# Kernel optimization log

Measured on AMD Instinct MI355X. Metric: run time of the kernel, lower is better.

## Reference

```python
import jax, jax.numpy as jnp
import numpy as np

LAYER_SIZES = [1024, 1024, 1024, 1024, 1024, 1024, 512]
MAX_PATHS = 128
BATCH = 128
N_LAYERS = len(LAYER_SIZES) - 1


def setup_inputs() -> dict:
    key = jax.random.key(0)
    keys = jax.random.split(key, 1 + 2 * N_LAYERS)
    inp = {"x": jax.random.normal(keys[0], (BATCH, LAYER_SIZES[0]), dtype=jnp.float32)}
    for i in range(N_LAYERS):
        inp[f"W{i}"] = jax.random.normal(keys[1 + 2 * i], (LAYER_SIZES[i], LAYER_SIZES[i + 1]), dtype=jnp.float32) * 0.01
        inp[f"b{i}"] = jax.random.normal(keys[2 + 2 * i], (LAYER_SIZES[i + 1],), dtype=jnp.float32) * 0.01
    return inp


def _layer(data, W, b):
    # data: [B, in_feat, P] -> [B, out_feat, 3P]
    B, _, P = data.shape
    O = W.shape[1]
    pos = jnp.einsum('bfp,fo->bpo', data, W) + b          # [B, P, O]; neg branch is exactly -pos
    branches = jnp.stack([-pos, jnp.zeros_like(pos), pos], axis=-1)  # [B, P, O, 3]
    # transpose(1,2) then reshape: interleave branches per source path, matching torch
    return branches.transpose(0, 2, 1, 3).reshape(B, O, P * 3)


def _prune(data, keep):
    # keep top-`keep` paths by L2 norm over the feature dim
    norms = jnp.linalg.norm(data, axis=1)                 # [B, P]
    _, idx = jax.lax.top_k(norms, keep)                   # [B, keep]
    return jnp.take_along_axis(data, idx[:, None, :], axis=-1)


def _forward(x, Ws, bs):
    data = x[:, :, None]                                   # [B, F, 1]
    for i in range(N_LAYERS):
        data = _layer(data, Ws[i], bs[i])
        if i < N_LAYERS - 1:
            data = jnp.tanh(data)
        if data.shape[-1] > MAX_PATHS:
            data = _prune(data, MAX_PATHS)
    # collapse with 'max_abs': per (batch, feature) pick path with largest |value|
    idx = jnp.argmax(jnp.abs(data), axis=-1, keepdims=True)
    output = jnp.take_along_axis(data, idx, axis=-1).squeeze(-1)
    return output, data


def reference(x, W0, b0, W1, b1, W2, b2, W3, b3, W4, b4, W5, b5):
    Ws = [W0, W1, W2, W3, W4, W5]
    bs = [b0, b1, b2, b3, b4, b5]
    return _forward(x, Ws, bs)
```

## Files before the change

### kernel.cpp

```cpp
#include <hip/hip_runtime.h>
#include <math.h>


using s8v = __attribute__((ext_vector_type(8))) short;
using f4v = __attribute__((ext_vector_type(4))) float;

__device__ __forceinline__ float bf2f(short b) {
  unsigned u = ((unsigned)(unsigned short)b) << 16;
  return __builtin_bit_cast(float, u);
}
__device__ __forceinline__ short f2bf(float f) {
  unsigned u = __builtin_bit_cast(unsigned, f);
  u = (u + 0x7FFFu + ((u >> 16) & 1u)) >> 16;
  return (short)u;
}
__device__ __forceinline__ void split_store(float f, short* hi, short* lo) {
  short h = f2bf(f);
  *hi = h;
  *lo = f2bf(f - bf2f(h));
}

__global__ void __launch_bounds__(256)
packx_k(const float* __restrict__ x, short* __restrict__ hi,
        short* __restrict__ lo) {
  int i = (blockIdx.x * 256 + threadIdx.x) * 4;
  float4 v = *(const float4*)&x[i];
  short4 h, l;
  h.x = f2bf(v.x); l.x = f2bf(v.x - bf2f(h.x));
  h.y = f2bf(v.y); l.y = f2bf(v.y - bf2f(h.y));
  h.z = f2bf(v.z); l.z = f2bf(v.z - bf2f(h.z));
  h.w = f2bf(v.w); l.w = f2bf(v.w - bf2f(h.w));
  *(short4*)&hi[i] = h;
  *(short4*)&lo[i] = l;
}

struct TWArgs {
  const float* W[6];
  short* Th[6];
  short* Tl[6];
};
__global__ void __launch_bounds__(256)
transW_all(TWArgs a) {
  const int z = blockIdx.z;
  const int N = (z == 5) ? 512 : 1024;
  const int n0 = blockIdx.x * 64, k0 = blockIdx.y * 64;
  if (n0 >= N) return;
  const float* __restrict__ W = a.W[z];
  short* __restrict__ Th = a.Th[z];
  short* __restrict__ Tl = a.Tl[z];
  __shared__ float tile[64][65];
  const int t = threadIdx.x;
  const int r = t >> 4, c4 = (t & 15) * 4;
#pragma unroll
  for (int i = 0; i < 4; ++i) {
    int rr = r + 16 * i;
    float4 v = *(const float4*)&W[(size_t)(k0 + rr) * N + n0 + c4];
    tile[rr][c4 + 0] = v.x;
    tile[rr][c4 + 1] = v.y;
    tile[rr][c4 + 2] = v.z;
    tile[rr][c4 + 3] = v.w;
  }
  __syncthreads();
#pragma unroll
  for (int i = 0; i < 4; ++i) {
    int n = r + 16 * i;
    short4 h, l;
    float f0 = tile[c4 + 0][n], f1 = tile[c4 + 1][n];
    float f2 = tile[c4 + 2][n], f3 = tile[c4 + 3][n];
    h.x = f2bf(f0); l.x = f2bf(f0 - bf2f(h.x));
    h.y = f2bf(f1); l.y = f2bf(f1 - bf2f(h.y));
    h.z = f2bf(f2); l.z = f2bf(f2 - bf2f(h.z));
    h.w = f2bf(f3); l.w = f2bf(f3 - bf2f(h.w));
    size_t o = (size_t)(n0 + n) * 1024 + k0 + c4;
    *(short4*)&Th[o] = h;
    *(short4*)&Tl[o] = l;
  }
}

template <int MODE, int D, int KS>
__global__ void __launch_bounds__(256, 2)
mfma_gemm(const short* __restrict__ Ah, const short* __restrict__ Al,
          const short* __restrict__ Bh, const short* __restrict__ Bl,
          const float* __restrict__ bias, short* __restrict__ Oh,
          short* __restrict__ Ol, float* __restrict__ Of, int N, int Dn) {
  constexpr int KC = 1024 / KS;
  constexpr int BKP = 40;
  __shared__ short As_h[64 * BKP], As_l[64 * BKP];
  __shared__ short Bs_h[64 * BKP], Bs_l[64 * BKP];
  const int t = threadIdx.x;
  const int row0 = blockIdx.y * 64;
  const int col0 = blockIdx.x * 64;
  const int kb = blockIdx.z * KC;
  const int sr = t >> 2, sko = (t & 3) * 8;
  const short* Ahp = Ah + (size_t)(row0 + sr) * 1024 + kb + sko;
  const short* Alp = Al + (size_t)(row0 + sr) * 1024 + kb + sko;
  const short* Bhp = Bh + (size_t)(col0 + sr) * 1024 + kb + sko;
  const short* Blp = Bl + (size_t)(col0 + sr) * 1024 + kb + sko;
  const int w = t >> 6, lane = t & 63;
  const int l16 = lane & 15, q = lane >> 4;
  const int wm0 = (w & 1) * 32, wn0 = (w >> 1) * 32;
  const int abase = (wm0 + l16) * BKP + q * 8;
  const int bbase = (wn0 + l16) * BKP + q * 8;
  f4v acc[2][2];
#pragma unroll
  for (int i = 0; i < 2; ++i)
#pragma unroll
    for (int j = 0; j < 2; ++j) acc[i][j] = (f4v){0.f, 0.f, 0.f, 0.f};
  uint4 rah = *(const uint4*)(Ahp);
  uint4 ral = *(const uint4*)(Alp);
  uint4 rbh = *(const uint4*)(Bhp);
  uint4 rbl = *(const uint4*)(Blp);
  for (int k0 = 0; k0 < KC; k0 += 32) {
    __syncthreads();
    *(uint4*)&As_h[sr * BKP + sko] = rah;
    *(uint4*)&As_l[sr * BKP + sko] = ral;
    *(uint4*)&Bs_h[sr * BKP + sko] = rbh;
    *(uint4*)&Bs_l[sr * BKP + sko] = rbl;
    if (k0 + 32 < KC) {
      rah = *(const uint4*)(Ahp + k0 + 32);
      ral = *(const uint4*)(Alp + k0 + 32);
      rbh = *(const uint4*)(Bhp + k0 + 32);
      rbl = *(const uint4*)(Blp + k0 + 32);
    }
    __syncthreads();
    s8v ah[2], al[2], bh[2], bl[2];
#pragma unroll
    for (int mt = 0; mt < 2; ++mt) {
      ah[mt] = *(const s8v*)&As_h[abase + mt * 16 * BKP];
      al[mt] = *(const s8v*)&As_l[abase + mt * 16 * BKP];
    }
#pragma unroll
    for (int nt = 0; nt < 2; ++nt) {
      bh[nt] = *(const s8v*)&Bs_h[bbase + nt * 16 * BKP];
      bl[nt] = *(const s8v*)&Bs_l[bbase + nt * 16 * BKP];
    }
#pragma unroll
    for (int mt = 0; mt < 2; ++mt)
#pragma unroll
      for (int nt = 0; nt < 2; ++nt) {
        acc[mt][nt] = __builtin_amdgcn_mfma_f32_16x16x32_bf16(
            ah[mt], bh[nt], acc[mt][nt], 0, 0, 0);
        acc[mt][nt] = __builtin_amdgcn_mfma_f32_16x16x32_bf16(
            ah[mt], bl[nt], acc[mt][nt], 0, 0, 0);
        acc[mt][nt] = __builtin_amdgcn_mfma_f32_16x16x32_bf16(
            al[mt], bh[nt], acc[mt][nt], 0, 0, 0);
      }
  }
  const int R = (int)gridDim.y << 6;
#pragma unroll
  for (int nt = 0; nt < 2; ++nt) {
    int gcol = col0 + wn0 + nt * 16 + l16;
    float bc = (MODE == 1) ? bias[gcol] : 0.f;
#pragma unroll
    for (int mt = 0; mt < 2; ++mt) {
#pragma unroll
      for (int r = 0; r < 4; ++r) {
        float v = acc[mt][nt][r];
        int rr = row0 + wm0 + mt * 16 + q * 4 + r;
        if (MODE == 1) {
          int b = rr / D, u = rr - b * D;
          size_t ob = (size_t)(b * Dn) * N + gcol;
          size_t om = ob + (size_t)(1 + 2 * u) * N;
          size_t op = ob + (size_t)(2 + 2 * u) * N;
          split_store(tanhf(bc - v), &Oh[om], &Ol[om]);
          split_store(tanhf(bc + v), &Oh[op], &Ol[op]);
          if (u == 0) split_store(tanhf(bc), &Oh[ob], &Ol[ob]);
        } else if (MODE == 2) {
          Of[(size_t)rr * N + gcol] = v;
        } else {
          Of[((size_t)blockIdx.z * R + rr) * N + gcol] = v;
        }
      }
    }
  }
}

template <int KS>
__global__ void __launch_bounds__(256)
comb0_hl(const float* __restrict__ P, const float* __restrict__ bias,
         short* __restrict__ Oh, short* __restrict__ Ol, int R, int N) {
  int i = blockIdx.x * 256 + threadIdx.x;
  int n4 = N >> 2;
  int r = i / n4, c4 = (i - r * n4) * 4;
  float4 y = *(const float4*)&P[(size_t)r * N + c4];
  size_t stride = (size_t)R * N;
#pragma unroll
  for (int ks = 1; ks < KS; ++ks) {
    const float4 p = *(const float4*)&P[ks * stride + (size_t)r * N + c4];
    y.x += p.x; y.y += p.y; y.z += p.z; y.w += p.w;
  }
  float4 bc = *(const float4*)(bias + c4);
  float t0 = tanhf(bc.x + y.x), t1 = tanhf(bc.y + y.y);
  float t2 = tanhf(bc.z + y.z), t3 = tanhf(bc.w + y.w);
  short4 h, l;
  h.x = f2bf(t0); l.x = f2bf(t0 - bf2f(h.x));
  h.y = f2bf(t1); l.y = f2bf(t1 - bf2f(h.y));
  h.z = f2bf(t2); l.z = f2bf(t2 - bf2f(h.z));
  h.w = f2bf(t3); l.w = f2bf(t3 - bf2f(h.w));
  *(short4*)&Oh[(size_t)r * N + c4] = h;
  *(short4*)&Ol[(size_t)r * N + c4] = l;
}

template <int KS, int D>
__global__ void __launch_bounds__(256)
comb1_hl(const float* __restrict__ P, const float* __restrict__ bias,
         short* __restrict__ Oh, short* __restrict__ Ol, int R, int N,
         int Dn) {
  int i = blockIdx.x * 256 + threadIdx.x;
  int n4 = N >> 2;
  int r = i / n4, c4 = (i - r * n4) * 4;
  int b = r / D, u = r - b * D;
  float4 y = *(const float4*)&P[(size_t)r * N + c4];
  size_t stride = (size_t)R * N;
#pragma unroll
  for (int ks = 1; ks < KS; ++ks) {
    const float4 p = *(const float4*)&P[ks * stride + (size_t)r * N + c4];
    y.x += p.x; y.y += p.y; y.z += p.z; y.w += p.w;
  }
  float4 bc = *(const float4*)(bias + c4);
  size_t ob = (size_t)(b * Dn) * N + c4;
  size_t om = ob + (size_t)(1 + 2 * u) * N;
  size_t op = ob + (size_t)(2 + 2 * u) * N;
  {
    float t0 = tanhf(bc.x - y.x), t1 = tanhf(bc.y - y.y);
    float t2 = tanhf(bc.z - y.z), t3 = tanhf(bc.w - y.w);
    short4 h, l;
    h.x = f2bf(t0); l.x = f2bf(t0 - bf2f(h.x));
    h.y = f2bf(t1); l.y = f2bf(t1 - bf2f(h.y));
    h.z = f2bf(t2); l.z = f2bf(t2 - bf2f(h.z));
    h.w = f2bf(t3); l.w = f2bf(t3 - bf2f(h.w));
    *(short4*)&Oh[om] = h;
    *(short4*)&Ol[om] = l;
  }
  {
    float t0 = tanhf(bc.x + y.x), t1 = tanhf(bc.y + y.y);
    float t2 = tanhf(bc.z + y.z), t3 = tanhf(bc.w + y.w);
    short4 h, l;
    h.x = f2bf(t0); l.x = f2bf(t0 - bf2f(h.x));
    h.y = f2bf(t1); l.y = f2bf(t1 - bf2f(h.y));
    h.z = f2bf(t2); l.z = f2bf(t2 - bf2f(h.z));
    h.w = f2bf(t3); l.w = f2bf(t3 - bf2f(h.w));
    *(short4*)&Oh[op] = h;
    *(short4*)&Ol[op] = l;
  }
  if (u == 0) {
    float t0 = tanhf(bc.x), t1 = tanhf(bc.y);
    float t2 = tanhf(bc.z), t3 = tanhf(bc.w);
    short4 h, l;
    h.x = f2bf(t0); l.x = f2bf(t0 - bf2f(h.x));
    h.y = f2bf(t1); l.y = f2bf(t1 - bf2f(h.y));
    h.z = f2bf(t2); l.z = f2bf(t2 - bf2f(h.z));
    h.w = f2bf(t3); l.w = f2bf(t3 - bf2f(h.w));
    *(short4*)&Oh[ob] = h;
    *(short4*)&Ol[ob] = l;
  }
}

__global__ void __launch_bounds__(256)
rownorm_hl(const short* __restrict__ hi, const short* __restrict__ lo,
           float* __restrict__ ns) {
  int row = blockIdx.x;
  int t = threadIdx.x;
  size_t base = (size_t)row * 1024 + t * 4;
  short4 h = *(const short4*)&hi[base];
  short4 l = *(const short4*)&lo[base];
  float v0 = bf2f(h.x) + bf2f(l.x);
  float v1 = bf2f(h.y) + bf2f(l.y);
  float v2 = bf2f(h.z) + bf2f(l.z);
  float v3 = bf2f(h.w) + bf2f(l.w);
  float s = v0 * v0 + v1 * v1 + v2 * v2 + v3 * v3;
  __shared__ float red[256];
  red[t] = s;
  __syncthreads();
  for (int off = 128; off; off >>= 1) {
    if (t < off) red[t] += red[t + off];
    __syncthreads();
  }
  if (t == 0) ns[row] = red[0];
}

__global__ void __launch_bounds__(256)
prune4_k(const float* __restrict__ ns, int* __restrict__ kept4) {
  int b = blockIdx.x, t = threadIdx.x;
  __shared__ float nss[31];
  __shared__ float key[243];
  __shared__ int cls[243];
  if (t < 31) nss[t] = ns[b * 31 + t];
  __syncthreads();
  if (t < 243) {
    int j = t / 3, t4 = t - 3 * j;
    int d0 = j / 27, d1 = (j / 9) % 3, d2 = (j / 3) % 3, d3 = j % 3;
    int u = 0;
    u = (d0 == 1) ? 0 : (1 + 2 * u + (d0 == 2));
    u = (d1 == 1) ? 0 : (1 + 2 * u + (d1 == 2));
    u = (d2 == 1) ? 0 : (1 + 2 * u + (d2 == 2));
    u = (d3 == 1) ? 0 : (1 + 2 * u + (d3 == 2));
    cls[t] = u;
    key[t] = (t4 == 1) ? 0.f : nss[u];
  }
  __syncthreads();
  if (t < 243) {
    float k = key[t];
    int rank = 0;
    for (int e = 0; e < 243; ++e) {
      float ke = key[e];
      rank += (ke > k) || (ke == k && e < t);
    }
    if (rank < 128) {
      int t4 = t - 3 * (t / 3);
      kept4[b * 128 + rank] = (cls[t] << 1) | (t4 == 2 ? 1 : 0);
    }
  }
}

__global__ void __launch_bounds__(256)
stats5_k(const float* __restrict__ Y5, const float* __restrict__ b5,
         float* __restrict__ dotv, float* __restrict__ nrmv,
         float* __restrict__ nb5) {
  int row = blockIdx.x;
  int t = threadIdx.x;
  __shared__ float rd[256], rn[256];
  if (row < 3968) {
    const float* y = Y5 + (size_t)row * 512;
    float d = 0.f, n2 = 0.f;
    for (int o = t; o < 512; o += 256) {
      float v = y[o];
      d = fmaf(b5[o], v, d);
      n2 = fmaf(v, v, n2);
    }
    rd[t] = d;
    rn[t] = n2;
    __syncthreads();
    for (int off = 128; off; off >>= 1) {
      if (t < off) {
        rd[t] += rd[t + off];
        rn[t] += rn[t + off];
      }
      __syncthreads();
    }
    if (t == 0) {
      dotv[row] = rd[0];
      nrmv[row] = rn[0];
    }
  } else {
    float n2 = 0.f;
    for (int o = t; o < 512; o += 256) {
      float v = b5[o];
      n2 = fmaf(v, v, n2);
    }
    rn[t] = n2;
    __syncthreads();
    for (int off = 128; off; off >>= 1) {
      if (t < off) rn[t] += rn[t + off];
      __syncthreads();
    }
    if (t == 0) nb5[0] = rn[0];
  }
}

__global__ void __launch_bounds__(384)
prune5_k(const float* __restrict__ dotv, const float* __restrict__ nrmv,
         const float* __restrict__ nb5, const int* __restrict__ kept4,
         int* __restrict__ kept5) {
  int b = blockIdx.x, t = threadIdx.x;
  __shared__ float pns[128];
  __shared__ float key[384];
  if (t < 128) {
    int k4 = kept4[b * 128 + t];
    int c = k4 >> 1;
    float s = (k4 & 1) ? 1.f : -1.f;
    pns[t] = nb5[0] + nrmv[b * 31 + c] + s * 2.f * dotv[b * 31 + c];
  }
  __syncthreads();
  int m = t / 3, tt = t - 3 * m;
  key[t] = (tt == 1) ? 0.f : pns[m];
  __syncthreads();
  float k = key[t];
  int rank = 0;
  for (int e = 0; e < 384; ++e) {
    float ke = key[e];
    rank += (ke > k) || (ke == k && e < t);
  }
  if (rank < 128) kept5[b * 128 + rank] = (m << 1) | (tt == 2 ? 1 : 0);
}

__global__ void __launch_bounds__(256)
finalize_k(const float* __restrict__ Y5, const float* __restrict__ b5,
           const int* __restrict__ kept4, const int* __restrict__ kept5,
           float* __restrict__ out, float* __restrict__ dataout) {
  const int b = blockIdx.y;
  const int o0 = blockIdx.x * 64;
  __shared__ float Ys[31][65];
  __shared__ float bias_s[64];
  __shared__ float vt[64][130];
  __shared__ float ra[64][4];
  __shared__ float rv[64][4];
  const int t = threadIdx.x;
  for (int idx = t; idx < 31 * 64; idx += 256) {
    int c = idx >> 6, o = idx & 63;
    Ys[c][o] = Y5[((size_t)b * 31 + c) * 512 + o0 + o];
  }
  if (t < 64) bias_s[t] = b5[o0 + t];
  const int rr = t & 127, oh = t >> 7;
  int k5 = kept5[b * 128 + rr];
  int m = k5 >> 1;
  float sig = (k5 & 1) ? 1.f : -1.f;
  int k4 = kept4[b * 128 + m];
  int cc = k4 >> 1;
  float s4 = (k4 & 1) ? 1.f : -1.f;
  float afac = sig * s4;
  __syncthreads();
#pragma unroll
  for (int ol = 0; ol < 32; ++ol) {
    int o = oh * 32 + ol;
    float v = sig * bias_s[o] + afac * Ys[cc][o];
    dataout[((size_t)b * 512 + o0 + o) * 128 + rr] = v;
    vt[o][rr] = v;
  }
  __syncthreads();
  int o = t >> 2, q = t & 3;
  float bestv = vt[o][q * 32];
  float besta = fabsf(bestv);
  for (int i = 1; i < 32; ++i) {
    float v = vt[o][q * 32 + i];
    float a = fabsf(v);
    if (a > besta) {
      besta = a;
      bestv = v;
    }
  }
  ra[o][q] = besta;
  rv[o][q] = bestv;
  __syncthreads();
  if (t < 64) {
    float ba = ra[t][0], bv = rv[t][0];
#pragma unroll
    for (int qq = 1; qq < 4; ++qq) {
      if (ra[t][qq] > ba) {
        ba = ra[t][qq];
        bv = rv[t][qq];
      }
    }
    out[(size_t)b * 512 + o0 + t] = bv;
  }
}

extern "C" void kernel_launch(void* const* d_in, const int* in_sizes, int n_in,
                              void* d_out, int out_size, void* d_ws,
                              size_t ws_size, hipStream_t stream) {
  const float* x = (const float*)d_in[0];
  const float* Wt[6];
  const float* bs[6];
  for (int i = 0; i < 6; ++i) {
    Wt[i] = (const float*)d_in[1 + 2 * i];
    bs[i] = (const float*)d_in[2 + 2 * i];
  }
  char* base = (char*)d_ws;
  short* A0h = (short*)(base + 0);
  short* A0l = (short*)(base + 262144);
  short* Wh[6], *Wl[6];
  {
    size_t off = 524288;
    for (int i = 0; i < 6; ++i) {
      size_t sz = (i < 5) ? 2097152 : 1048576;
      Wh[i] = (short*)(base + off);
      Wl[i] = (short*)(base + off + sz);
      off += 2 * sz;
    }
  }
  short* C1h = (short*)(base + 23592960), *C1l = (short*)(base + 23855104);
  short* C2h = (short*)(base + 24117248), *C2l = (short*)(base + 24903680);
  short* C3h = (short*)(base + 25690112), *C3l = (short*)(base + 27525120);
  short* C4h = (short*)(base + 29360128), *C4l = (short*)(base + 33292288);
  short* C5h = (short*)(base + 524288);
  short* C5l = (short*)(base + 8912896);
  float* PA = (float*)(base + 29360128);
  float* PB = (float*)(base + 524288);
  float* Y5 = (float*)(base + 23592960);
  float* ns = (float*)(base + 37224448);
  float* dotv = (float*)(base + 37240320);
  float* nrmv = (float*)(base + 37256192);
  float* nb5 = (float*)(base + 37272064);
  int* kept4 = (int*)(base + 37272068);
  int* kept5 = (int*)(base + 37337604);
  float* outp = (float*)d_out;
  float* dataout = outp + 128 * 512;

  dim3 blk(256);
  packx_k<<<dim3(128), blk, 0, stream>>>(x, A0h, A0l);
  TWArgs twa;
  for (int i = 0; i < 6; ++i) {
    twa.W[i] = Wt[i];
    twa.Th[i] = Wh[i];
    twa.Tl[i] = Wl[i];
  }
  transW_all<<<dim3(16, 16, 6), blk, 0, stream>>>(twa);

  mfma_gemm<3, 1, 4><<<dim3(16, 2, 4), blk, 0, stream>>>(
      A0h, A0l, Wh[0], Wl[0], nullptr, nullptr, nullptr, PA, 1024, 0);
  comb0_hl<4><<<dim3(128), blk, 0, stream>>>(PA, bs[0], C1h, C1l, 128, 1024);
  mfma_gemm<3, 1, 4><<<dim3(16, 2, 4), blk, 0, stream>>>(
      C1h, C1l, Wh[1], Wl[1], nullptr, nullptr, nullptr, PA, 1024, 0);
  comb1_hl<4, 1><<<dim3(128), blk, 0, stream>>>(PA, bs[1], C2h, C2l, 128, 1024,
                                                3);
  mfma_gemm<3, 3, 4><<<dim3(16, 6, 4), blk, 0, stream>>>(
      C2h, C2l, Wh[2], Wl[2], nullptr, nullptr, nullptr, PA, 1024, 0);
  comb1_hl<4, 3><<<dim3(384), blk, 0, stream>>>(PA, bs[2], C3h, C3l, 384, 1024,
                                                7);
  mfma_gemm<3, 7, 2><<<dim3(16, 14, 2), blk, 0, stream>>>(
      C3h, C3l, Wh[3], Wl[3], nullptr, nullptr, nullptr, PB, 1024, 0);
  comb1_hl<2, 7><<<dim3(896), blk, 0, stream>>>(PB, bs[3], C4h, C4l, 896, 1024,
                                                15);
  mfma_gemm<1, 15, 1><<<dim3(16, 30), blk, 0, stream>>>(
      C4h, C4l, Wh[4], Wl[4], bs[4], C5h, C5l, nullptr, 1024, 31);
  rownorm_hl<<<dim3(3968), blk, 0, stream>>>(C5h, C5l, ns);
  prune4_k<<<dim3(128), blk, 0, stream>>>(ns, kept4);
  mfma_gemm<2, 31, 1><<<dim3(8, 62), blk, 0, stream>>>(
      C5h, C5l, Wh[5], Wl[5], nullptr, nullptr, nullptr, Y5, 512, 0);
  stats5_k<<<dim3(3969), blk, 0, stream>>>(Y5, bs[5], dotv, nrmv, nb5);
  prune5_k<<<dim3(128), dim3(384), 0, stream>>>(dotv, nrmv, nb5, kept4, kept5);
  finalize_k<<<dim3(8, 128), blk, 0, stream>>>(Y5, bs[5], kept4, kept5, outp,
                                               dataout);
}
```

Baseline: 243.1 us.

## Fuse split-K reductions, row norms and stats into GEMM epilogues

Folds the x packing and zeroing of counters/accumulators into the weight-transpose launch. Split-K partial reductions with bias+tanh+hi/lo split now run inside the GEMM, done by the last-arriving block per tile via an atomic counter; layer 0/1 split-K is raised to 8. Row norms and the layer-5 dot/norm stats are computed in the GEMM epilogues with shuffle reductions and float atomics, and the two prune kernels are merged into one. This removes about seven launches and their intermediate global round trips, at the cost of atomics, thread fences and nondeterministic float summation order.

Result: slower. 421.3 us (+73.3%).

```diff
diff --git a/kernel.cpp b/kernel.cpp
--- a/kernel.cpp
+++ b/kernel.cpp
@@ -18,20 +18,6 @@
   short h = f2bf(f);
   *hi = h;
   *lo = f2bf(f - bf2f(h));
-}
-
-__global__ void __launch_bounds__(256)
-packx_k(const float* __restrict__ x, short* __restrict__ hi,
-        short* __restrict__ lo) {
-  int i = (blockIdx.x * 256 + threadIdx.x) * 4;
-  float4 v = *(const float4*)&x[i];
-  short4 h, l;
-  h.x = f2bf(v.x); l.x = f2bf(v.x - bf2f(h.x));
-  h.y = f2bf(v.y); l.y = f2bf(v.y - bf2f(h.y));
-  h.z = f2bf(v.z); l.z = f2bf(v.z - bf2f(h.z));
-  h.w = f2bf(v.w); l.w = f2bf(v.w - bf2f(h.w));
-  *(short4*)&hi[i] = h;
-  *(short4*)&lo[i] = l;
 }
 
 struct TWArgs {
@@ -40,7 +26,31 @@
   short* Tl[6];
 };
 __global__ void __launch_bounds__(256)
-transW_all(TWArgs a) {
+transW_all(TWArgs a, const float* __restrict__ x, short* __restrict__ A0h,
+           short* __restrict__ A0l, float4* __restrict__ zreg) {
+  __shared__ float tile[64][65];
+  const int t = threadIdx.x;
+  if (blockIdx.z == 6) {
+    const int bf = blockIdx.y * 16 + blockIdx.x;
+    if (bf < 128) {
+      int i = (bf * 256 + t) * 4;
+      float4 v = *(const float4*)&x[i];
+      short4 h, l;
+      h.x = f2bf(v.x); l.x = f2bf(v.x - bf2f(h.x));
+      h.y = f2bf(v.y); l.y = f2bf(v.y - bf2f(h.y));
+      h.z = f2bf(v.z); l.z = f2bf(v.z - bf2f(h.z));
+      h.w = f2bf(v.w); l.w = f2bf(v.w - bf2f(h.w));
+      *(short4*)&A0h[i] = h;
+      *(short4*)&A0l[i] = l;
+    } else {
+      int flat = (bf - 128) * 256 + t;
+      if (flat < 3168) {
+        float4 zz = {0.f, 0.f, 0.f, 0.f};
+        zreg[flat] = zz;
+      }
+    }
+    return;
+  }
   const int z = blockIdx.z;
   const int N = (z == 5) ? 512 : 1024;
   const int n0 = blockIdx.x * 64, k0 = blockIdx.y * 64;
@@ -48,8 +58,6 @@
   const float* __restrict__ W = a.W[z];
   short* __restrict__ Th = a.Th[z];
   short* __restrict__ Tl = a.Tl[z];
-  __shared__ float tile[64][65];
-  const int t = threadIdx.x;
   const int r = t >> 4, c4 = (t & 15) * 4;
 #pragma unroll
   for (int i = 0; i < 4; ++i) {
@@ -82,7 +90,9 @@
 mfma_gemm(const short* __restrict__ Ah, const short* __restrict__ Al,
           const short* __restrict__ Bh, const short* __restrict__ Bl,
           const float* __restrict__ bias, short* __restrict__ Oh,
-          short* __restrict__ Ol, float* __restrict__ Of, int N, int Dn) {
+          short* __restrict__ Ol, float* __restrict__ Of,
+          float* __restrict__ aux0, float* __restrict__ aux1,
+          int* __restrict__ cnt, int N, int Dn) {
   constexpr int KC = 1024 / KS;
   constexpr int BKP = 40;
   __shared__ short As_h[64 * BKP], As_l[64 * BKP];
@@ -147,146 +157,194 @@
       }
   }
   const int R = (int)gridDim.y << 6;
+
+  if (MODE == 1) {
+    const float bc0 = bias[col0 + wn0 + l16];
+    const float bc1 = bias[col0 + wn0 + 16 + l16];
+#pragma unroll
+    for (int mt = 0; mt < 2; ++mt) {
+#pragma unroll
+      for (int r = 0; r < 4; ++r) {
+        const int rr = row0 + wm0 + mt * 16 + q * 4 + r;
+        const int b = rr / D, u = rr - b * D;
+        const size_t obr = (size_t)(b * Dn) * N;
+        const size_t omr = obr + (size_t)(1 + 2 * u) * N;
+        const size_t opr = obr + (size_t)(2 + 2 * u) * N;
+        float sm = 0.f, sp = 0.f, sb = 0.f;
+#pragma unroll
+        for (int nt = 0; nt < 2; ++nt) {
+          const int gcol = col0 + wn0 + nt * 16 + l16;
+          const float bc = nt ? bc1 : bc0;
+          const float v = acc[mt][nt][r];
+          float tm = tanhf(bc - v), tp = tanhf(bc + v);
+          split_store(tm, &Oh[omr + gcol], &Ol[omr + gcol]);
+          split_store(tp, &Oh[opr + gcol], &Ol[opr + gcol]);
+          sm = fmaf(tm, tm, sm);
+          sp = fmaf(tp, tp, sp);
+          if (u == 0) {
+            float tb = tanhf(bc);
+            split_store(tb, &Oh[obr + gcol], &Ol[obr + gcol]);
+            sb = fmaf(tb, tb, sb);
+          }
+        }
+#pragma unroll
+        for (int d = 1; d < 16; d <<= 1) {
+          sm += __shfl_xor(sm, d);
+          sp += __shfl_xor(sp, d);
+          sb += __shfl_xor(sb, d);
+        }
+        if (l16 == 0) {
+          atomicAdd(&aux0[b * Dn + 1 + 2 * u], sm);
+          atomicAdd(&aux0[b * Dn + 2 + 2 * u], sp);
+          if (u == 0) atomicAdd(&aux0[b * Dn], sb);
+        }
+      }
+    }
+    return;
+  }
+
+  if (MODE == 2) {
+    const float bc0 = bias[col0 + wn0 + l16];
+    const float bc1 = bias[col0 + wn0 + 16 + l16];
+#pragma unroll
+    for (int mt = 0; mt < 2; ++mt) {
+#pragma unroll
+      for (int r = 0; r < 4; ++r) {
+        const int rr = row0 + wm0 + mt * 16 + q * 4 + r;
+        float sd = 0.f, sn = 0.f;
+#pragma unroll
+        for (int nt = 0; nt < 2; ++nt) {
+          const int gcol = col0 + wn0 + nt * 16 + l16;
+          const float bc = nt ? bc1 : bc0;
+          const float v = acc[mt][nt][r];
+          Of[(size_t)rr * N + gcol] = v;
+          sd = fmaf(bc, v, sd);
+          sn = fmaf(v, v, sn);
+        }
+#pragma unroll
+        for (int d = 1; d < 16; d <<= 1) {
+          sd += __shfl_xor(sd, d);
+          sn += __shfl_xor(sn, d);
+        }
+        if (l16 == 0) {
+          atomicAdd(&aux0[rr], sd);
+          atomicAdd(&aux1[rr], sn);
+        }
+      }
+    }
+    return;
+  }
+
 #pragma unroll
   for (int nt = 0; nt < 2; ++nt) {
     int gcol = col0 + wn0 + nt * 16 + l16;
-    float bc = (MODE == 1) ? bias[gcol] : 0.f;
-#pragma unroll
-    for (int mt = 0; mt < 2; ++mt) {
+#pragma unroll
+    for (int mt = 0; mt < 2; ++mt)
 #pragma unroll
       for (int r = 0; r < 4; ++r) {
-        float v = acc[mt][nt][r];
         int rr = row0 + wm0 + mt * 16 + q * 4 + r;
-        if (MODE == 1) {
-          int b = rr / D, u = rr - b * D;
-          size_t ob = (size_t)(b * Dn) * N + gcol;
-          size_t om = ob + (size_t)(1 + 2 * u) * N;
-          size_t op = ob + (size_t)(2 + 2 * u) * N;
-          split_store(tanhf(bc - v), &Oh[om], &Ol[om]);
-          split_store(tanhf(bc + v), &Oh[op], &Ol[op]);
-          if (u == 0) split_store(tanhf(bc), &Oh[ob], &Ol[ob]);
-        } else if (MODE == 2) {
-          Of[(size_t)rr * N + gcol] = v;
-        } else {
-          Of[((size_t)blockIdx.z * R + rr) * N + gcol] = v;
-        }
-      }
-    }
-  }
-}
-
-template <int KS>
-__global__ void __launch_bounds__(256)
-comb0_hl(const float* __restrict__ P, const float* __restrict__ bias,
-         short* __restrict__ Oh, short* __restrict__ Ol, int R, int N) {
-  int i = blockIdx.x * 256 + threadIdx.x;
-  int n4 = N >> 2;
-  int r = i / n4, c4 = (i - r * n4) * 4;
-  float4 y = *(const float4*)&P[(size_t)r * N + c4];
-  size_t stride = (size_t)R * N;
-#pragma unroll
-  for (int ks = 1; ks < KS; ++ks) {
-    const float4 p = *(const float4*)&P[ks * stride + (size_t)r * N + c4];
-    y.x += p.x; y.y += p.y; y.z += p.z; y.w += p.w;
-  }
-  float4 bc = *(const float4*)(bias + c4);
-  float t0 = tanhf(bc.x + y.x), t1 = tanhf(bc.y + y.y);
-  float t2 = tanhf(bc.z + y.z), t3 = tanhf(bc.w + y.w);
-  short4 h, l;
-  h.x = f2bf(t0); l.x = f2bf(t0 - bf2f(h.x));
-  h.y = f2bf(t1); l.y = f2bf(t1 - bf2f(h.y));
-  h.z = f2bf(t2); l.z = f2bf(t2 - bf2f(h.z));
-  h.w = f2bf(t3); l.w = f2bf(t3 - bf2f(h.w));
-  *(short4*)&Oh[(size_t)r * N + c4] = h;
-  *(short4*)&Ol[(size_t)r * N + c4] = l;
-}
-
-template <int KS, int D>
-__global__ void __launch_bounds__(256)
-comb1_hl(const float* __restrict__ P, const float* __restrict__ bias,
-         short* __restrict__ Oh, short* __restrict__ Ol, int R, int N,
-         int Dn) {
-  int i = blockIdx.x * 256 + threadIdx.x;
-  int n4 = N >> 2;
-  int r = i / n4, c4 = (i - r * n4) * 4;
-  int b = r / D, u = r - b * D;
-  float4 y = *(const float4*)&P[(size_t)r * N + c4];
-  size_t stride = (size_t)R * N;
-#pragma unroll
-  for (int ks = 1; ks < KS; ++ks) {
-    const float4 p = *(const float4*)&P[ks * stride + (size_t)r * N + c4];
-    y.x += p.x; y.y += p.y; y.z += p.z; y.w += p.w;
-  }
-  float4 bc = *(const float4*)(bias + c4);
-  size_t ob = (size_t)(b * Dn) * N + c4;
-  size_t om = ob + (size_t)(1 + 2 * u) * N;
-  size_t op = ob + (size_t)(2 + 2 * u) * N;
-  {
-    float t0 = tanhf(bc.x - y.x), t1 = tanhf(bc.y - y.y);
-    float t2 = tanhf(bc.z - y.z), t3 = tanhf(bc.w - y.w);
-    short4 h, l;
-    h.x = f2bf(t0); l.x = f2bf(t0 - bf2f(h.x));
-    h.y = f2bf(t1); l.y = f2bf(t1 - bf2f(h.y));
-    h.z = f2bf(t2); l.z = f2bf(t2 - bf2f(h.z));
-    h.w = f2bf(t3); l.w = f2bf(t3 - bf2f(h.w));
-    *(short4*)&Oh[om] = h;
-    *(short4*)&Ol[om] = l;
-  }
-  {
-    float t0 = tanhf(bc.x + y.x), t1 = tanhf(bc.y + y.y);
-    float t2 = tanhf(bc.z + y.z), t3 = tanhf(bc.w + y.w);
-    short4 h, l;
-    h.x = f2bf(t0); l.x = f2bf(t0 - bf2f(h.x));
-    h.y = f2bf(t1); l.y = f2bf(t1 - bf2f(h.y));
-    h.z = f2bf(t2); l.z = f2bf(t2 - bf2f(h.z));
-    h.w = f2bf(t3); l.w = f2bf(t3 - bf2f(h.w));
-    *(short4*)&Oh[op] = h;
-    *(short4*)&Ol[op] = l;
-  }
-  if (u == 0) {
-    float t0 = tanhf(bc.x), t1 = tanhf(bc.y);
-    float t2 = tanhf(bc.z), t3 = tanhf(bc.w);
-    short4 h, l;
-    h.x = f2bf(t0); l.x = f2bf(t0 - bf2f(h.x));
-    h.y = f2bf(t1); l.y = f2bf(t1 - bf2f(h.y));
-    h.z = f2bf(t2); l.z = f2bf(t2 - bf2f(h.z));
-    h.w = f2bf(t3); l.w = f2bf(t3 - bf2f(h.w));
-    *(short4*)&Oh[ob] = h;
-    *(short4*)&Ol[ob] = l;
-  }
-}
-
-__global__ void __launch_bounds__(256)
-rownorm_hl(const short* __restrict__ hi, const short* __restrict__ lo,
-           float* __restrict__ ns) {
-  int row = blockIdx.x;
-  int t = threadIdx.x;
-  size_t base = (size_t)row * 1024 + t * 4;
-  short4 h = *(const short4*)&hi[base];
-  short4 l = *(const short4*)&lo[base];
-  float v0 = bf2f(h.x) + bf2f(l.x);
-  float v1 = bf2f(h.y) + bf2f(l.y);
-  float v2 = bf2f(h.z) + bf2f(l.z);
-  float v3 = bf2f(h.w) + bf2f(l.w);
-  float s = v0 * v0 + v1 * v1 + v2 * v2 + v3 * v3;
-  __shared__ float red[256];
-  red[t] = s;
+        Of[((size_t)blockIdx.z * R + rr) * N + gcol] = acc[mt][nt][r];
+      }
+  }
+  __threadfence();
+  __syncthreads();
+  __shared__ int lastf;
+  if (t == 0) {
+    int tile = blockIdx.y * gridDim.x + blockIdx.x;
+    lastf = (atomicAdd(&cnt[tile], 1) == KS - 1);
+  }
+  __syncthreads();
+  if (!lastf) return;
+  __threadfence();
+  const size_t pstride = (size_t)R * N;
+  for (int it = 0; it < 4; ++it) {
+    const int slot = it * 256 + t;
+    const int lr = slot >> 4, c4 = (slot & 15) << 2;
+    const int rr = row0 + lr;
+    const size_t off = (size_t)rr * N + col0 + c4;
+    float4 y = *(const float4*)&Of[off];
+#pragma unroll
+    for (int ks = 1; ks < KS; ++ks) {
+      const float4 p = *(const float4*)&Of[ks * pstride + off];
+      y.x += p.x; y.y += p.y; y.z += p.z; y.w += p.w;
+    }
+    const float4 bc = *(const float4*)&bias[col0 + c4];
+    if (MODE == 6) {
+      float t0 = tanhf(bc.x + y.x), t1 = tanhf(bc.y + y.y);
+      float t2 = tanhf(bc.z + y.z), t3 = tanhf(bc.w + y.w);
+      size_t o = (size_t)rr * N + col0 + c4;
+      short4 h, l;
+      h.x = f2bf(t0); l.x = f2bf(t0 - bf2f(h.x));
+      h.y = f2bf(t1); l.y = f2bf(t1 - bf2f(h.y));
+      h.z = f2bf(t2); l.z = f2bf(t2 - bf2f(h.z));
+      h.w = f2bf(t3); l.w = f2bf(t3 - bf2f(h.w));
+      *(short4*)&Oh[o] = h;
+      *(short4*)&Ol[o] = l;
+    } else {
+      const int b = rr / D, u = rr - b * D;
+      const size_t ob = (size_t)(b * Dn) * N + col0 + c4;
+      const size_t om = ob + (size_t)(1 + 2 * u) * N;
+      const size_t op = ob + (size_t)(2 + 2 * u) * N;
+      {
+        float t0 = tanhf(bc.x - y.x), t1 = tanhf(bc.y - y.y);
+        float t2 = tanhf(bc.z - y.z), t3 = tanhf(bc.w - y.w);
+        short4 h, l;
+        h.x = f2bf(t0); l.x = f2bf(t0 - bf2f(h.x));
+        h.y = f2bf(t1); l.y = f2bf(t1 - bf2f(h.y));
+        h.z = f2bf(t2); l.z = f2bf(t2 - bf2f(h.z));
+        h.w = f2bf(t3); l.w = f2bf(t3 - bf2f(h.w));
+        *(short4*)&Oh[om] = h;
+        *(short4*)&Ol[om] = l;
+      }
+      {
+        float t0 = tanhf(bc.x + y.x), t1 = tanhf(bc.y + y.y);
+        float t2 = tanhf(bc.z + y.z), t3 = tanhf(bc.w + y.w);
+        short4 h, l;
+        h.x = f2bf(t0); l.x = f2bf(t0 - bf2f(h.x));
+        h.y = f2bf(t1); l.y = f2bf(t1 - bf2f(h.y));
+        h.z = f2bf(t2); l.z = f2bf(t2 - bf2f(h.z));
+        h.w = f2bf(t3); l.w = f2bf(t3 - bf2f(h.w));
+        *(short4*)&Oh[op] = h;
+        *(short4*)&Ol[op] = l;
+      }
+      if (u == 0) {
+        float t0 = tanhf(bc.x), t1 = tanhf(bc.y);
+        float t2 = tanhf(bc.z), t3 = tanhf(bc.w);
+        short4 h, l;
+        h.x = f2bf(t0); l.x = f2bf(t0 - bf2f(h.x));
+        h.y = f2bf(t1); l.y = f2bf(t1 - bf2f(h.y));
+        h.z = f2bf(t2); l.z = f2bf(t2 - bf2f(h.z));
+        h.w = f2bf(t3); l.w = f2bf(t3 - bf2f(h.w));
+        *(short4*)&Oh[ob] = h;
+        *(short4*)&Ol[ob] = l;
+      }
+    }
+  }
+}
+
+__global__ void __launch_bounds__(384)
+prune45_k(const float* __restrict__ ns, const float* __restrict__ dotv,
+          const float* __restrict__ nrmv, const float* __restrict__ b5,
+          int* __restrict__ kept4, int* __restrict__ kept5) {
+  const int b = blockIdx.x, t = threadIdx.x;
+  __shared__ float nss[31];
+  __shared__ float rb[256];
+  __shared__ float keyA[243];
+  __shared__ int cls[243];
+  __shared__ int k4s[128];
+  __shared__ float pns[128];
+  __shared__ float keyB[384];
+  if (t < 31) nss[t] = ns[b * 31 + t];
+  if (t < 256) {
+    float a = b5[t], c = b5[t + 256];
+    rb[t] = a * a + c * c;
+  }
   __syncthreads();
   for (int off = 128; off; off >>= 1) {
-    if (t < off) red[t] += red[t + off];
+    if (t < off) rb[t] += rb[t + off];
     __syncthreads();
   }
-  if (t == 0) ns[row] = red[0];
-}
-
-__global__ void __launch_bounds__(256)
-prune4_k(const float* __restrict__ ns, int* __restrict__ kept4) {
-  int b = blockIdx.x, t = threadIdx.x;
-  __shared__ float nss[31];
-  __shared__ float key[243];
-  __shared__ int cls[243];
-  if (t < 31) nss[t] = ns[b * 31 + t];
-  __syncthreads();
+  const float nb5 = rb[0];
   if (t < 243) {
     int j = t / 3, t4 = t - 3 * j;
     int d0 = j / 27, d1 = (j / 9) % 3, d2 = (j / 3) % 3, d3 = j % 3;
@@ -296,89 +354,38 @@
     u = (d2 == 1) ? 0 : (1 + 2 * u + (d2 == 2));
     u = (d3 == 1) ? 0 : (1 + 2 * u + (d3 == 2));
     cls[t] = u;
-    key[t] = (t4 == 1) ? 0.f : nss[u];
+    keyA[t] = (t4 == 1) ? 0.f : nss[u];
   }
   __syncthreads();
   if (t < 243) {
-    float k = key[t];
+    float k = keyA[t];
     int rank = 0;
     for (int e = 0; e < 243; ++e) {
-      float ke = key[e];
+      float ke = keyA[e];
       rank += (ke > k) || (ke == k && e < t);
     }
     if (rank < 128) {
       int t4 = t - 3 * (t / 3);
-      kept4[b * 128 + rank] = (cls[t] << 1) | (t4 == 2 ? 1 : 0);
-    }
-  }
-}
-
-__global__ void __launch_bounds__(256)
-stats5_k(const float* __restrict__ Y5, const float* __restrict__ b5,
-         float* __restrict__ dotv, float* __restrict__ nrmv,
-         float* __restrict__ nb5) {
-  int row = blockIdx.x;
-  int t = threadIdx.x;
-  __shared__ float rd[256], rn[256];
-  if (row < 3968) {
-    const float* y = Y5 + (size_t)row * 512;
-    float d = 0.f, n2 = 0.f;
-    for (int o = t; o < 512; o += 256) {
-      float v = y[o];
-      d = fmaf(b5[o], v, d);
-      n2 = fmaf(v, v, n2);
-    }
-    rd[t] = d;
-    rn[t] = n2;
-    __syncthreads();
-    for (int off = 128; off; off >>= 1) {
-      if (t < off) {
-        rd[t] += rd[t + off];
-        rn[t] += rn[t + off];
-      }
-      __syncthreads();
-    }
-    if (t == 0) {
-      dotv[row] = rd[0];
-      nrmv[row] = rn[0];
-    }
-  } else {
-    float n2 = 0.f;
-    for (int o = t; o < 512; o += 256) {
-      float v = b5[o];
-      n2 = fmaf(v, v, n2);
-    }
-    rn[t] = n2;
-    __syncthreads();
-    for (int off = 128; off; off >>= 1) {
-      if (t < off) rn[t] += rn[t + off];
-      __syncthreads();
-    }
-    if (t == 0) nb5[0] = rn[0];
-  }
-}
-
-__global__ void __launch_bounds__(384)
-prune5_k(const float* __restrict__ dotv, const float* __restrict__ nrmv,
-         const float* __restrict__ nb5, const int* __restrict__ kept4,
-         int* __restrict__ kept5) {
-  int b = blockIdx.x, t = threadIdx.x;
-  __shared__ float pns[128];
-  __shared__ float key[384];
+      int kv = (cls[t] << 1) | (t4 == 2 ? 1 : 0);
+      k4s[rank] = kv;
+      kept4[b * 128 + rank] = kv;
+    }
+  }
+  __syncthreads();
   if (t < 128) {
-    int k4 = kept4[b * 128 + t];
+    int k4 = k4s[t];
     int c = k4 >> 1;
     float s = (k4 & 1) ? 1.f : -1.f;
-    pns[t] = nb5[0] + nrmv[b * 31 + c] + s * 2.f * dotv[b * 31 + c];
-  }
-  __syncthreads();
-  int m = t / 3, tt = t - 3 * m;
-  key[t] = (tt == 1) ? 0.f : pns[m];
-  __syncthreads();
-  float k = key[t];
+    pns[t] = nb5 + nrmv[b * 31 + c] + s * 2.f * dotv[b * 31 + c];
+  }
+  __syncthreads();
+  const int m = t / 3, tt = t - 3 * m;
+  keyB[t] = (tt == 1) ? 0.f : pns[m];
+  __syncthreads();
+  float k = keyB[t];
   int rank = 0;
   for (int e = 0; e < 384; ++e) {
-    float ke = key[e];
+    float ke = keyB[e];
     rank += (ke > k) || (ke == k && e < t);
   }
   if (rank < 128) kept5[b * 128 + rank] = (m << 1) | (tt == 2 ? 1 : 0);
@@ -477,48 +484,48 @@
   float* PA = (float*)(base + 29360128);
   float* PB = (float*)(base + 524288);
   float* Y5 = (float*)(base + 23592960);
-  float* ns = (float*)(base + 37224448);
-  float* dotv = (float*)(base + 37240320);
-  float* nrmv = (float*)(base + 37256192);
-  float* nb5 = (float*)(base + 37272064);
-  int* kept4 = (int*)(base + 37272068);
-  int* kept5 = (int*)(base + 37337604);
+  char* zb = base + 37224448;
+  int* cnt0 = (int*)zb;
+  int* cnt1 = cnt0 + 32;
+  int* cnt2 = cnt1 + 32;
+  int* cnt3 = cnt2 + 96;
+  float* ns = (float*)(zb + 1536);
+  float* dotv = (float*)(zb + 17408);
+  float* nrmv = (float*)(zb + 33280);
+  int* kept4 = (int*)(zb + 50688);
+  int* kept5 = (int*)(zb + 116224);
   float* outp = (float*)d_out;
   float* dataout = outp + 128 * 512;
 
   dim3 blk(256);
-  packx_k<<<dim3(128), blk, 0, stream>>>(x, A0h, A0l);
   TWArgs twa;
   for (int i = 0; i < 6; ++i) {
     twa.W[i] = Wt[i];
     twa.Th[i] = Wh[i];
     twa.Tl[i] = Wl[i];
   }
-  transW_all<<<dim3(16, 16, 6), blk, 0, stream>>>(twa);
-
-  mfma_gemm<3, 1, 4><<<dim3(16, 2, 4), blk, 0, stream>>>(
-      A0h, A0l, Wh[0], Wl[0], nullptr, nullptr, nullptr, PA, 1024, 0);
-  comb0_hl<4><<<dim3(128), blk, 0, stream>>>(PA, bs[0], C1h, C1l, 128, 1024);
-  mfma_gemm<3, 1, 4><<<dim3(16, 2, 4), blk, 0, stream>>>(
-      C1h, C1l, Wh[1], Wl[1], nullptr, nullptr, nullptr, PA, 1024, 0);
-  comb1_hl<4, 1><<<dim3(128), blk, 0, stream>>>(PA, bs[1], C2h, C2l, 128, 1024,
-                                                3);
-  mfma_gemm<3, 3, 4><<<dim3(16, 6, 4), blk, 0, stream>>>(
-      C2h, C2l, Wh[2], Wl[2], nullptr, nullptr, nullptr, PA, 1024, 0);
-  comb1_hl<4, 3><<<dim3(384), blk, 0, stream>>>(PA, bs[2], C3h, C3l, 384, 1024,
-                                                7);
-  mfma_gemm<3, 7, 2><<<dim3(16, 14, 2), blk, 0, stream>>>(
-      C3h, C3l, Wh[3], Wl[3], nullptr, nullptr, nullptr, PB, 1024, 0);
-  comb1_hl<2, 7><<<dim3(896), blk, 0, stream>>>(PB, bs[3], C4h, C4l, 896, 1024,
-                                                15);
+  transW_all<<<dim3(16, 16, 7), blk, 0, stream>>>(twa, x, A0h, A0l,
+                                                  (float4*)zb);
+  mfma_gemm<6, 1, 8><<<dim3(16, 2, 8), blk, 0, stream>>>(
+      A0h, A0l, Wh[0], Wl[0], bs[0], C1h, C1l, PA, nullptr, nullptr, cnt0,
+      1024, 0);
+  mfma_gemm<7, 1, 8><<<dim3(16, 2, 8), blk, 0, stream>>>(
+      C1h, C1l, Wh[1], Wl[1], bs[1], C2h, C2l, PA, nullptr, nullptr, cnt1,
+      1024, 3);
+  mfma_gemm<7, 3, 4><<<dim3(16, 6, 4), blk, 0, stream>>>(
+      C2h, C2l, Wh[2], Wl[2], bs[2], C3h, C3l, PA, nullptr, nullptr, cnt2,
+      1024, 7);
+  mfma_gemm<7, 7, 2><<<dim3(16, 14, 2), blk, 0, stream>>>(
+      C3h, C3l, Wh[3], Wl[3], bs[3], C4h, C4l, PB, nullptr, nullptr, cnt3,
+      1024, 15);
   mfma_gemm<1, 15, 1><<<dim3(16, 30), blk, 0, stream>>>(
-      C4h, C4l, Wh[4], Wl[4], bs[4], C5h, C5l, nullptr, 1024, 31);
-  rownorm_hl<<<dim3(3968), blk, 0, stream>>>(C5h, C5l, ns);
-  prune4_k<<<dim3(128), blk, 0, stream>>>(ns, kept4);
+      C4h, C4l, Wh[4], Wl[4], bs[4], C5h, C5l, nullptr, ns, nullptr, nullptr,
+      1024, 31);
   mfma_gemm<2, 31, 1><<<dim3(8, 62), blk, 0, stream>>>(
-      C5h, C5l, Wh[5], Wl[5], nullptr, nullptr, nullptr, Y5, 512, 0);
-  stats5_k<<<dim3(3969), blk, 0, stream>>>(Y5, bs[5], dotv, nrmv, nb5);
-  prune5_k<<<dim3(128), dim3(384), 0, stream>>>(dotv, nrmv, nb5, kept4, kept5);
+      C5h, C5l, Wh[5], Wl[5], bs[5], nullptr, nullptr, Y5, dotv, nrmv, nullptr,
+      512, 0);
+  prune45_k<<<dim3(128), dim3(384), 0, stream>>>(ns, dotv, nrmv, bs[5], kept4,
+                                                 kept5);
   finalize_k<<<dim3(8, 128), blk, 0, stream>>>(Y5, bs[5], kept4, kept5, outp,
                                                dataout);
 }
```
